# Kernel tuning notes

Measured on AMD Instinct MI355X. Metric: run time of the kernel, lower is better.

Reference implementation:

```python
import jax, jax.numpy as jnp
import numpy as np

N = 50000      # nodes
E = 800000     # edges (avg degree 16)
S = 2          # sample_size
D_IN = 128     # input_dim
D_NOISE = 64   # noise_dim
D0 = 256       # output_dims[0]
D1 = 256       # output_dims[1]


def setup_inputs() -> dict:
    key = jax.random.key(0)
    ks = jax.random.split(key, 8)
    X = jax.random.normal(ks[0], (1, N, D_IN), dtype=jnp.float32)
    edge_src = jax.random.randint(ks[1], (E,), 0, N)
    edge_dst = jax.random.randint(ks[2], (E,), 0, N)
    # Bernoulli(0.5) noise, as in torch.distributions.Bernoulli
    epsilon = (jax.random.uniform(ks[3], (S, N, D_NOISE)) < 0.5).astype(jnp.float32)
    W0 = jax.random.normal(ks[4], (D_IN + D_NOISE, D0), dtype=jnp.float32) * 0.05
    b0 = jnp.zeros((D0,), jnp.float32)
    W1 = jax.random.normal(ks[5], (D0, D1), dtype=jnp.float32) * 0.05
    b1 = jnp.zeros((D1,), jnp.float32)
    eps0 = jnp.zeros((), jnp.float32)  # GINConv learnable eps, init 0
    eps1 = jnp.zeros((), jnp.float32)
    return dict(X=X, epsilon=epsilon, edge_src=edge_src, edge_dst=edge_dst,
                W0=W0, b0=b0, W1=W1, b1=b1, eps0=eps0, eps1=eps1)


def reference(X, epsilon, edge_src, edge_dst, W0, b0, W1, b1, eps0, eps1):
    # Expand features over sample dim and concat noise: [S, N, D_IN + D_NOISE]
    feat = jnp.broadcast_to(X, (epsilon.shape[0], X.shape[1], X.shape[2]))
    h = jnp.concatenate([feat, epsilon], axis=2)

    def gin_layer(h, eps, W, b):
        # sum aggregation over in-edges: agg[:, d] += h[:, s] for each edge (s, d)
        agg = jnp.zeros_like(h).at[:, edge_dst, :].add(h[:, edge_src, :])
        return jax.nn.relu(((1.0 + eps) * h + agg) @ W + b)

    h = gin_layer(h, eps0, W0, b0)
    h = gin_layer(h, eps1, W1, b1)
    out = jax.nn.relu(h)  # outer activation applied once more in forward()
    return out, epsilon
```

## Files before the change

### kernel.cpp

```cpp
#include <hip/hip_runtime.h>
#include <hip/hip_bf16.h>

#define NN 50000
#define NE 800000
#define NS 2
#define DIN 128
#define DNOISE 64
#define DH0 192
#define DOUT 256
#define NB 49

typedef __bf16 bf16x8 __attribute__((ext_vector_type(8)));
typedef float floatx4 __attribute__((ext_vector_type(4)));


__device__ inline float bflo(unsigned int u) { return __uint_as_float(u << 16); }
__device__ inline float bfhi(unsigned int u) { return __uint_as_float(u & 0xffff0000u); }
__device__ inline unsigned short f2bf_bits(float x) {
    __hip_bfloat16 b = __float2bfloat16(x);
    return *reinterpret_cast<unsigned short*>(&b);
}
__device__ inline unsigned int pack2(float lo, float hi) {
    return (unsigned int)f2bf_bits(lo) | ((unsigned int)f2bf_bits(hi) << 16);
}


__global__ void count_kernel(const int* __restrict__ dst, int* __restrict__ cnt) {
    int i = blockIdx.x * blockDim.x + threadIdx.x;
    if (i < NE) atomicAdd(&cnt[dst[i]], 1);
}

__global__ __launch_bounds__(1024) void scanA_kernel(const int* __restrict__ cnt, int* __restrict__ bsum) {
    int i = blockIdx.x * 1024 + threadIdx.x;
    int v = (i < NN) ? cnt[i] : 0;
    for (int off = 32; off > 0; off >>= 1) v += __shfl_down(v, off);
    __shared__ int wsum[16];
    if ((threadIdx.x & 63) == 0) wsum[threadIdx.x >> 6] = v;
    __syncthreads();
    if (threadIdx.x == 0) {
        int s = 0;
        for (int k = 0; k < 16; ++k) s += wsum[k];
        bsum[blockIdx.x] = s;
    }
}

__global__ __launch_bounds__(64) void scanB_kernel(int* __restrict__ bsum) {
    int lane = threadIdx.x;
    int orig = (lane < NB) ? bsum[lane] : 0;
    int v = orig;
    for (int off = 1; off < 64; off <<= 1) {
        int t = __shfl_up(v, off);
        if (lane >= off) v += t;
    }
    if (lane < NB) bsum[lane] = v - orig;
}

__global__ __launch_bounds__(1024) void scanC_kernel(int* __restrict__ cnt, const int* __restrict__ bsum,
                                                     int* __restrict__ row_ptr) {
    __shared__ int buf[1024];
    int tid = threadIdx.x;
    int i = blockIdx.x * 1024 + tid;
    int v = (i < NN) ? cnt[i] : 0;
    buf[tid] = v;
    __syncthreads();
    for (int off = 1; off < 1024; off <<= 1) {
        int t = (tid >= off) ? buf[tid - off] : 0;
        __syncthreads();
        buf[tid] += t;
        __syncthreads();
    }
    int excl = buf[tid] - v + bsum[blockIdx.x];
    if (i < NN) { row_ptr[i + 1] = excl + v; cnt[i] = excl; }
    if (i == 0) row_ptr[0] = 0;
}

__global__ void fill_kernel(const int* __restrict__ src, const int* __restrict__ dst,
                            int* __restrict__ cursor, int* __restrict__ col_idx) {
    int i = blockIdx.x * blockDim.x + threadIdx.x;
    if (i < NE) {
        int p = atomicAdd(&cursor[dst[i]], 1);
        col_idx[p] = src[i];
    }
}

#define XQ (NN * DIN / 4)
#define XB4 ((XQ + 255) / 256)
#define NR_BLOCKS ((NS * NN + 255) / 256)

__global__ void prep_kernel(const float* __restrict__ X, unsigned short* __restrict__ Xb,
                            const float* __restrict__ noise, uint2* __restrict__ Nbit) {
    int b = blockIdx.x;
    if (b < XB4) {
        int i = b * 256 + threadIdx.x;
        if (i < XQ) {
            float4 v = reinterpret_cast<const float4*>(X)[i];
            ushort4 o;
            o.x = f2bf_bits(v.x); o.y = f2bf_bits(v.y); o.z = f2bf_bits(v.z); o.w = f2bf_bits(v.w);
            reinterpret_cast<ushort4*>(Xb)[i] = o;
        }
    } else {
        int r = (b - XB4) * 256 + threadIdx.x;
        if (r < NS * NN) {
            const float4* p = reinterpret_cast<const float4*>(noise + (size_t)r * DNOISE);
            unsigned int lo = 0, hi = 0;
            for (int q = 0; q < 8; ++q) {
                float4 v = p[q];
                int base = q * 4;
                lo |= (v.x != 0.f ? 1u : 0u) << base;
                lo |= (v.y != 0.f ? 1u : 0u) << (base + 1);
                lo |= (v.z != 0.f ? 1u : 0u) << (base + 2);
                lo |= (v.w != 0.f ? 1u : 0u) << (base + 3);
            }
            for (int q = 8; q < 16; ++q) {
                float4 v = p[q];
                int base = q * 4 - 32;
                hi |= (v.x != 0.f ? 1u : 0u) << base;
                hi |= (v.y != 0.f ? 1u : 0u) << (base + 1);
                hi |= (v.z != 0.f ? 1u : 0u) << (base + 2);
                hi |= (v.w != 0.f ? 1u : 0u) << (base + 3);
            }
            uint2 o; o.x = lo; o.y = hi;
            Nbit[r] = o;
        }
    }
}


__global__ void transpose_both(const float* __restrict__ W0, const float* __restrict__ W1,
                               __hip_bfloat16* __restrict__ Wt0, __hip_bfloat16* __restrict__ Wt1) {
    int b = blockIdx.x;
    if (b < DOUT) {
        for (int k = threadIdx.x; k < DH0; k += blockDim.x)
            Wt0[(size_t)b * DH0 + k] = __float2bfloat16(W0[(size_t)k * DOUT + b]);
    } else {
        int n = b - DOUT;
        for (int k = threadIdx.x; k < DOUT; k += blockDim.x)
            Wt1[(size_t)n * DOUT + k] = __float2bfloat16(W1[(size_t)k * DOUT + n]);
    }
}


__global__ __launch_bounds__(256) void agg0_kernel(
    const unsigned int* __restrict__ Xb,
    const uint2* __restrict__ Nbit,
    const int* __restrict__ row_ptr, const int* __restrict__ col_idx,
    const float* __restrict__ eps0p,
    unsigned int* __restrict__ z0) {
    const int d = blockIdx.x * 2 + (threadIdx.x >> 7);
    const int cc = threadIdx.x & 127;
    const float c = 1.f + eps0p[0];
    const int beg = row_ptr[d], end = row_ptr[d + 1];
    if (cc < 64) {
        const unsigned int* src = Xb + cc;
        unsigned int u = src[(size_t)d * 64];
        float aL = c * bflo(u), aH = c * bfhi(u);
        int e = beg;
        for (; e + 3 < end; e += 4) {
            int i0 = col_idx[e], i1 = col_idx[e + 1], i2 = col_idx[e + 2], i3 = col_idx[e + 3];
            unsigned int u0 = src[(size_t)i0 * 64], u1 = src[(size_t)i1 * 64];
            unsigned int u2 = src[(size_t)i2 * 64], u3 = src[(size_t)i3 * 64];
            aL += (bflo(u0) + bflo(u1)) + (bflo(u2) + bflo(u3));
            aH += (bfhi(u0) + bfhi(u1)) + (bfhi(u2) + bfhi(u3));
        }
        for (; e < end; ++e) {
            unsigned int ue = src[(size_t)col_idx[e] * 64];
            aL += bflo(ue); aH += bfhi(ue);
        }
        unsigned int r = pack2(aL, aH);
        z0[(size_t)d * 96 + cc] = r;
        z0[(size_t)(NN + d) * 96 + cc] = r;
    } else {
        int j = cc - 64;
        int s = j >> 5, col = j & 31;
        const uint2* src = Nbit + (size_t)s * NN;
        const int word = col >> 4;
        const int sh = (2 * col) & 31;
        uint2 uS = src[d];
        unsigned int wS = word ? uS.y : uS.x;
        int c0 = 0, c1 = 0;
        int e = beg;
        for (; e + 3 < end; e += 4) {
            uint2 u0 = src[col_idx[e]], u1 = src[col_idx[e + 1]];
            uint2 u2 = src[col_idx[e + 2]], u3 = src[col_idx[e + 3]];
            unsigned int w0 = word ? u0.y : u0.x, w1 = word ? u1.y : u1.x;
            unsigned int w2 = word ? u2.y : u2.x, w3 = word ? u3.y : u3.x;
            c0 += (int)((w0 >> sh) & 1) + (int)((w1 >> sh) & 1) + (int)((w2 >> sh) & 1) + (int)((w3 >> sh) & 1);
            c1 += (int)((w0 >> (sh + 1)) & 1) + (int)((w1 >> (sh + 1)) & 1) +
                  (int)((w2 >> (sh + 1)) & 1) + (int)((w3 >> (sh + 1)) & 1);
        }
        for (; e < end; ++e) {
            uint2 ue = src[col_idx[e]];
            unsigned int we = word ? ue.y : ue.x;
            c0 += (int)((we >> sh) & 1);
            c1 += (int)((we >> (sh + 1)) & 1);
        }
        float aL = c * (float)((wS >> sh) & 1) + (float)c0;
        float aH = c * (float)((wS >> (sh + 1)) & 1) + (float)c1;
        z0[(size_t)(s * NN + d) * 96 + 64 + col] = pack2(aL, aH);
    }
}


__global__ __launch_bounds__(256) void agg1_kernel(
    const uint2* __restrict__ h,
    const int* __restrict__ row_ptr, const int* __restrict__ col_idx,
    const float* __restrict__ eps1p,
    uint2* __restrict__ z1) {
    const int d = blockIdx.x * 2 + (threadIdx.x >> 7);
    const int s = (threadIdx.x >> 6) & 1;
    const int cc = threadIdx.x & 63;
    const float c = 1.f + eps1p[0];
    const int beg = row_ptr[d], end = row_ptr[d + 1];
    const uint2* src = h + (size_t)s * NN * 64 + cc;
    uint2 u = src[(size_t)d * 64];
    float aL0 = c * bflo(u.x), aH0 = c * bfhi(u.x);
    float aL1 = c * bflo(u.y), aH1 = c * bfhi(u.y);
    int e = beg;
    for (; e + 7 < end; e += 8) {
        uint2 g[8];
#pragma unroll
        for (int q = 0; q < 8; ++q) g[q] = src[(size_t)col_idx[e + q] * 64];
#pragma unroll
        for (int q = 0; q < 8; ++q) {
            aL0 += bflo(g[q].x); aH0 += bfhi(g[q].x);
            aL1 += bflo(g[q].y); aH1 += bfhi(g[q].y);
        }
    }
    for (; e + 3 < end; e += 4) {
        uint2 u0 = src[(size_t)col_idx[e] * 64], u1 = src[(size_t)col_idx[e + 1] * 64];
        uint2 u2 = src[(size_t)col_idx[e + 2] * 64], u3 = src[(size_t)col_idx[e + 3] * 64];
        aL0 += (bflo(u0.x) + bflo(u1.x)) + (bflo(u2.x) + bflo(u3.x));
        aH0 += (bfhi(u0.x) + bfhi(u1.x)) + (bfhi(u2.x) + bfhi(u3.x));
        aL1 += (bflo(u0.y) + bflo(u1.y)) + (bflo(u2.y) + bflo(u3.y));
        aH1 += (bfhi(u0.y) + bfhi(u1.y)) + (bfhi(u2.y) + bfhi(u3.y));
    }
    for (; e < end; ++e) {
        uint2 ue = src[(size_t)col_idx[e] * 64];
        aL0 += bflo(ue.x); aH0 += bfhi(ue.x);
        aL1 += bflo(ue.y); aH1 += bfhi(ue.y);
    }
    uint2 r; r.x = pack2(aL0, aH0); r.y = pack2(aL1, aH1);
    z1[(size_t)(s * NN + d) * 64 + cc] = r;
}


__device__ inline void store_out(float* C, size_t idx, float v) { C[idx] = v; }
__device__ inline void store_out(__hip_bfloat16* C, size_t idx, float v) { C[idx] = __float2bfloat16(v); }

template <typename OUT_T>
__global__ __launch_bounds__(256) void gemm_bias_relu(
    const __hip_bfloat16* __restrict__ A, const __hip_bfloat16* __restrict__ Wt,
    const float* __restrict__ bias, OUT_T* __restrict__ C,
    int M, int K) {
    const int lane = threadIdx.x & 63;
    const int wave = threadIdx.x >> 6;
    const int rowBase = blockIdx.x * 128 + wave * 32;
    if (rowBase >= M) return;
    const int lo = lane & 15;
    const int quad = lane >> 4;

    floatx4 acc0[16], acc1[16];
#pragma unroll
    for (int t = 0; t < 16; ++t) {
        acc0[t] = (floatx4){0.f, 0.f, 0.f, 0.f};
        acc1[t] = (floatx4){0.f, 0.f, 0.f, 0.f};
    }

    const __hip_bfloat16* arow0 = A + (size_t)(rowBase + lo) * K + quad * 8;
    const __hip_bfloat16* arow1 = arow0 + (size_t)16 * K;
    for (int k0 = 0; k0 < K; k0 += 32) {
        bf16x8 a0 = *reinterpret_cast<const bf16x8*>(arow0 + k0);
        bf16x8 a1 = *reinterpret_cast<const bf16x8*>(arow1 + k0);
#pragma unroll
        for (int t = 0; t < 16; ++t) {
            bf16x8 b = *reinterpret_cast<const bf16x8*>(Wt + (size_t)(t * 16 + lo) * K + k0 + quad * 8);
            acc0[t] = __builtin_amdgcn_mfma_f32_16x16x32_bf16(a0, b, acc0[t], 0, 0, 0);
            acc1[t] = __builtin_amdgcn_mfma_f32_16x16x32_bf16(a1, b, acc1[t], 0, 0, 0);
        }
    }

#pragma unroll
    for (int t = 0; t < 16; ++t) {
        int col = t * 16 + lo;
        float bv = bias[col];
#pragma unroll
        for (int r = 0; r < 4; ++r) {
            int row0 = rowBase + quad * 4 + r;
            float v0 = acc0[t][r] + bv;
            store_out(C, (size_t)row0 * DOUT + col, v0 > 0.f ? v0 : 0.f);
            float v1 = acc1[t][r] + bv;
            store_out(C, (size_t)(row0 + 16) * DOUT + col, v1 > 0.f ? v1 : 0.f);
        }
    }
}


__global__ void copy_eps(const uint4* __restrict__ src, uint4* __restrict__ dst) {
    int i = blockIdx.x * blockDim.x + threadIdx.x;
    const int n16 = (NS * NN * DNOISE * 4) / 16;
    if (i < n16) dst[i] = src[i];
}

extern "C" void kernel_launch(void* const* d_in, const int* in_sizes, int n_in,
                              void* d_out, int out_size, void* d_ws, size_t ws_size,
                              hipStream_t stream) {
    const float* X = (const float*)d_in[0];
    const float* noise = (const float*)d_in[1];
    const int* esrc = (const int*)d_in[2];
    const int* edst = (const int*)d_in[3];
    const float* W0 = (const float*)d_in[4];
    const float* b0 = (const float*)d_in[5];
    const float* W1 = (const float*)d_in[6];
    const float* b1 = (const float*)d_in[7];
    const float* eps0 = (const float*)d_in[8];
    const float* eps1 = (const float*)d_in[9];
    float* out = (float*)d_out;

    const int M = NS * NN;

    char* w = (char*)d_ws;
    auto carve = [&](size_t bytes) { char* p = w; w += (bytes + 511) & ~(size_t)511; return p; };
    int* cursor = (int*)carve((size_t)NN * 4);
    int* row_ptr = (int*)carve((size_t)(NN + 1) * 4);
    int* col_idx = (int*)carve((size_t)NE * 4);
    int* bsum = (int*)carve((size_t)NB * 4);
    uint2* Nbit = (uint2*)carve((size_t)M * 8);
    __hip_bfloat16* Wt0 = (__hip_bfloat16*)carve((size_t)DH0 * DOUT * 2);
    __hip_bfloat16* Wt1 = (__hip_bfloat16*)carve((size_t)DOUT * DOUT * 2);
    unsigned int* z = (unsigned int*)carve((size_t)M * DOUT * 2);

    __hip_bfloat16* h1 = (__hip_bfloat16*)d_out;
    unsigned short* Xb = (unsigned short*)(out + (size_t)M * DOUT);

    hipMemsetAsync(cursor, 0, (size_t)NN * 4, stream);
    count_kernel<<<(NE + 255) / 256, 256, 0, stream>>>(edst, cursor);
    scanA_kernel<<<NB, 1024, 0, stream>>>(cursor, bsum);
    scanB_kernel<<<1, 64, 0, stream>>>(bsum);
    scanC_kernel<<<NB, 1024, 0, stream>>>(cursor, bsum, row_ptr);
    fill_kernel<<<(NE + 255) / 256, 256, 0, stream>>>(esrc, edst, cursor, col_idx);
    prep_kernel<<<XB4 + NR_BLOCKS, 256, 0, stream>>>(X, Xb, noise, Nbit);
    transpose_both<<<2 * DOUT, 256, 0, stream>>>(W0, W1, Wt0, Wt1);

    agg0_kernel<<<NN / 2, 256, 0, stream>>>(
        (const unsigned int*)Xb, Nbit, row_ptr, col_idx, eps0, z);
    gemm_bias_relu<__hip_bfloat16><<<(M + 127) / 128, 256, 0, stream>>>(
        (const __hip_bfloat16*)z, Wt0, b0, h1, M, DH0);
    agg1_kernel<<<NN / 2, 256, 0, stream>>>(
        (const uint2*)h1, row_ptr, col_idx, eps1, (uint2*)z);
    gemm_bias_relu<float><<<(M + 127) / 128, 256, 0, stream>>>(
        (const __hip_bfloat16*)z, Wt1, b1, out, M, DOUT);

    copy_eps<<<((NS * NN * DNOISE * 4 / 16) + 255) / 256, 256, 0, stream>>>(
        (const uint4*)noise, (uint4*)(out + (size_t)M * DOUT));
}
```

Measured before the change: 610.0 us.

## Interleave sample rows in h1 for wider agg1 gathers and fuse epsilon copy

The first GEMM now writes its output node-major with the two sample rows interleaved, so one agg1 gather fetches 16-byte words covering both samples of a source node. Each wave then handles a whole node, with the edge range made wave-uniform via readfirstlane, and agg1 launches half as many blocks. The epsilon passthrough copy is folded into prep_kernel, and the bf16 X staging buffer moves into workspace so the output region is not overwritten. This cuts gather transactions and drops one kernel launch, at the cost of a less regular store pattern in the first GEMM.

```diff
diff --git a/kernel.cpp b/kernel.cpp
--- a/kernel.cpp
+++ b/kernel.cpp
@@ -88,7 +88,8 @@
 #define NR_BLOCKS ((NS * NN + 255) / 256)
 
 __global__ void prep_kernel(const float* __restrict__ X, unsigned short* __restrict__ Xb,
-                            const float* __restrict__ noise, uint2* __restrict__ Nbit) {
+                            const float* __restrict__ noise, uint2* __restrict__ Nbit,
+                            float* __restrict__ out_eps) {
     int b = blockIdx.x;
     if (b < XB4) {
         int i = b * 256 + threadIdx.x;
@@ -102,9 +103,11 @@
         int r = (b - XB4) * 256 + threadIdx.x;
         if (r < NS * NN) {
             const float4* p = reinterpret_cast<const float4*>(noise + (size_t)r * DNOISE);
+            float4* oe = reinterpret_cast<float4*>(out_eps + (size_t)r * DNOISE);
             unsigned int lo = 0, hi = 0;
             for (int q = 0; q < 8; ++q) {
                 float4 v = p[q];
+                oe[q] = v;
                 int base = q * 4;
                 lo |= (v.x != 0.f ? 1u : 0u) << base;
                 lo |= (v.y != 0.f ? 1u : 0u) << (base + 1);
@@ -113,6 +116,7 @@
             }
             for (int q = 8; q < 16; ++q) {
                 float4 v = p[q];
+                oe[q] = v;
                 int base = q * 4 - 32;
                 hi |= (v.x != 0.f ? 1u : 0u) << base;
                 hi |= (v.y != 0.f ? 1u : 0u) << (base + 1);
@@ -202,52 +206,66 @@
 
 
 __global__ __launch_bounds__(256) void agg1_kernel(
-    const uint2* __restrict__ h,
+    const uint4* __restrict__ h,
     const int* __restrict__ row_ptr, const int* __restrict__ col_idx,
     const float* __restrict__ eps1p,
-    uint2* __restrict__ z1) {
-    const int d = blockIdx.x * 2 + (threadIdx.x >> 7);
-    const int s = (threadIdx.x >> 6) & 1;
-    const int cc = threadIdx.x & 63;
+    uint4* __restrict__ z1) {
+    const int d = blockIdx.x * 4 + (threadIdx.x >> 6);
+    const int lane = threadIdx.x & 63;
     const float c = 1.f + eps1p[0];
-    const int beg = row_ptr[d], end = row_ptr[d + 1];
-    const uint2* src = h + (size_t)s * NN * 64 + cc;
-    uint2 u = src[(size_t)d * 64];
-    float aL0 = c * bflo(u.x), aH0 = c * bfhi(u.x);
-    float aL1 = c * bflo(u.y), aH1 = c * bfhi(u.y);
+    const int beg = __builtin_amdgcn_readfirstlane(row_ptr[d]);
+    const int end = __builtin_amdgcn_readfirstlane(row_ptr[d + 1]);
+    const uint4* src = h + lane;
+    uint4 u = src[(size_t)d * 64];
+    float a0 = c * bflo(u.x), a1 = c * bfhi(u.x);
+    float a2 = c * bflo(u.y), a3 = c * bfhi(u.y);
+    float a4 = c * bflo(u.z), a5 = c * bfhi(u.z);
+    float a6 = c * bflo(u.w), a7 = c * bfhi(u.w);
     int e = beg;
     for (; e + 7 < end; e += 8) {
-        uint2 g[8];
+        uint4 g[8];
 #pragma unroll
         for (int q = 0; q < 8; ++q) g[q] = src[(size_t)col_idx[e + q] * 64];
 #pragma unroll
         for (int q = 0; q < 8; ++q) {
-            aL0 += bflo(g[q].x); aH0 += bfhi(g[q].x);
-            aL1 += bflo(g[q].y); aH1 += bfhi(g[q].y);
-        }
-    }
-    for (; e + 3 < end; e += 4) {
-        uint2 u0 = src[(size_t)col_idx[e] * 64], u1 = src[(size_t)col_idx[e + 1] * 64];
-        uint2 u2 = src[(size_t)col_idx[e + 2] * 64], u3 = src[(size_t)col_idx[e + 3] * 64];
-        aL0 += (bflo(u0.x) + bflo(u1.x)) + (bflo(u2.x) + bflo(u3.x));
-        aH0 += (bfhi(u0.x) + bfhi(u1.x)) + (bfhi(u2.x) + bfhi(u3.x));
-        aL1 += (bflo(u0.y) + bflo(u1.y)) + (bflo(u2.y) + bflo(u3.y));
-        aH1 += (bfhi(u0.y) + bfhi(u1.y)) + (bfhi(u2.y) + bfhi(u3.y));
+            a0 += bflo(g[q].x); a1 += bfhi(g[q].x);
+            a2 += bflo(g[q].y); a3 += bfhi(g[q].y);
+            a4 += bflo(g[q].z); a5 += bfhi(g[q].z);
+            a6 += bflo(g[q].w); a7 += bfhi(g[q].w);
+        }
+    }
+    if (e + 3 < end) {
+        uint4 g[4];
+#pragma unroll
+        for (int q = 0; q < 4; ++q) g[q] = src[(size_t)col_idx[e + q] * 64];
+#pragma unroll
+        for (int q = 0; q < 4; ++q) {
+            a0 += bflo(g[q].x); a1 += bfhi(g[q].x);
+            a2 += bflo(g[q].y); a3 += bfhi(g[q].y);
+            a4 += bflo(g[q].z); a5 += bfhi(g[q].z);
+            a6 += bflo(g[q].w); a7 += bfhi(g[q].w);
+        }
+        e += 4;
     }
     for (; e < end; ++e) {
-        uint2 ue = src[(size_t)col_idx[e] * 64];
-        aL0 += bflo(ue.x); aH0 += bfhi(ue.x);
-        aL1 += bflo(ue.y); aH1 += bfhi(ue.y);
-    }
-    uint2 r; r.x = pack2(aL0, aH0); r.y = pack2(aL1, aH1);
-    z1[(size_t)(s * NN + d) * 64 + cc] = r;
+        uint4 ge = src[(size_t)col_idx[e] * 64];
+        a0 += bflo(ge.x); a1 += bfhi(ge.x);
+        a2 += bflo(ge.y); a3 += bfhi(ge.y);
+        a4 += bflo(ge.z); a5 += bfhi(ge.z);
+        a6 += bflo(ge.w); a7 += bfhi(ge.w);
+    }
+    const int s = lane >> 5, q = lane & 31;
+    uint4 r;
+    r.x = pack2(a0, a1); r.y = pack2(a2, a3);
+    r.z = pack2(a4, a5); r.w = pack2(a6, a7);
+    z1[(size_t)(s * NN + d) * 32 + q] = r;
 }
 
 
 __device__ inline void store_out(float* C, size_t idx, float v) { C[idx] = v; }
 __device__ inline void store_out(__hip_bfloat16* C, size_t idx, float v) { C[idx] = __float2bfloat16(v); }
 
-template <typename OUT_T>
+template <bool SWZ, typename OUT_T>
 __global__ __launch_bounds__(256) void gemm_bias_relu(
     const __hip_bfloat16* __restrict__ A, const __hip_bfloat16* __restrict__ Wt,
     const float* __restrict__ bias, OUT_T* __restrict__ C,
@@ -285,20 +303,16 @@
         float bv = bias[col];
 #pragma unroll
         for (int r = 0; r < 4; ++r) {
-            int row0 = rowBase + quad * 4 + r;
+            int m0 = rowBase + quad * 4 + r;
+            int m1 = m0 + 16;
+            size_t o0 = SWZ ? ((m0 < NN) ? (size_t)m0 * 2 : (size_t)(m0 - NN) * 2 + 1) : (size_t)m0;
+            size_t o1 = SWZ ? ((m1 < NN) ? (size_t)m1 * 2 : (size_t)(m1 - NN) * 2 + 1) : (size_t)m1;
             float v0 = acc0[t][r] + bv;
-            store_out(C, (size_t)row0 * DOUT + col, v0 > 0.f ? v0 : 0.f);
+            store_out(C, o0 * DOUT + col, v0 > 0.f ? v0 : 0.f);
             float v1 = acc1[t][r] + bv;
-            store_out(C, (size_t)(row0 + 16) * DOUT + col, v1 > 0.f ? v1 : 0.f);
-        }
-    }
-}
-
-
-__global__ void copy_eps(const uint4* __restrict__ src, uint4* __restrict__ dst) {
-    int i = blockIdx.x * blockDim.x + threadIdx.x;
-    const int n16 = (NS * NN * DNOISE * 4) / 16;
-    if (i < n16) dst[i] = src[i];
+            store_out(C, o1 * DOUT + col, v1 > 0.f ? v1 : 0.f);
+        }
+    }
 }
 
 extern "C" void kernel_launch(void* const* d_in, const int* in_sizes, int n_in,
@@ -330,7 +344,7 @@
     unsigned int* z = (unsigned int*)carve((size_t)M * DOUT * 2);
 
     __hip_bfloat16* h1 = (__hip_bfloat16*)d_out;
-    unsigned short* Xb = (unsigned short*)(out + (size_t)M * DOUT);
+    unsigned short* Xb = (unsigned short*)(z + (size_t)M * 96);
 
     hipMemsetAsync(cursor, 0, (size_t)NN * 4, stream);
     count_kernel<<<(NE + 255) / 256, 256, 0, stream>>>(edst, cursor);
@@ -338,18 +352,16 @@
     scanB_kernel<<<1, 64, 0, stream>>>(bsum);
     scanC_kernel<<<NB, 1024, 0, stream>>>(cursor, bsum, row_ptr);
     fill_kernel<<<(NE + 255) / 256, 256, 0, stream>>>(esrc, edst, cursor, col_idx);
-    prep_kernel<<<XB4 + NR_BLOCKS, 256, 0, stream>>>(X, Xb, noise, Nbit);
+    prep_kernel<<<XB4 + NR_BLOCKS, 256, 0, stream>>>(X, Xb, noise, Nbit,
+                                                     out + (size_t)M * DOUT);
     transpose_both<<<2 * DOUT, 256, 0, stream>>>(W0, W1, Wt0, Wt1);
 
     agg0_kernel<<<NN / 2, 256, 0, stream>>>(
         (const unsigned int*)Xb, Nbit, row_ptr, col_idx, eps0, z);
-    gemm_bias_relu<__hip_bfloat16><<<(M + 127) / 128, 256, 0, stream>>>(
+    gemm_bias_relu<true, __hip_bfloat16><<<(M + 127) / 128, 256, 0, stream>>>(
         (const __hip_bfloat16*)z, Wt0, b0, h1, M, DH0);
-    agg1_kernel<<<NN / 2, 256, 0, stream>>>(
-        (const uint2*)h1, row_ptr, col_idx, eps1, (uint2*)z);
-    gemm_bias_relu<float><<<(M + 127) / 128, 256, 0, stream>>>(
+    agg1_kernel<<<NN / 4, 256, 0, stream>>>(
+        (const uint4*)h1, row_ptr, col_idx, eps1, (uint4*)z);
+    gemm_bias_relu<false, float><<<(M + 127) / 128, 256, 0, stream>>>(
         (const __hip_bfloat16*)z, Wt1, b1, out, M, DOUT);
-
-    copy_eps<<<((NS * NN * DNOISE * 4 / 16) + 255) / 256, 256, 0, stream>>>(
-        (const uint4*)noise, (uint4*)(out + (size_t)M * DOUT));
-}
+}
```

Measured after the change: 660.6 us. 8.3% more time.
